# Kernel optimization log

Measured on AMD Instinct MI355X. Metric: run time of the kernel, lower is better.

## Reference

```python
import jax, jax.numpy as jnp
import numpy as np

EPS = 1e-5


def setup_inputs() -> dict:
    key = jax.random.key(0)
    ks = jax.random.split(key, 5)
    b, c, L = 2, 512, 1024
    x = jax.random.normal(ks[0], (b, c, L), dtype=jnp.float32)
    gamma = jnp.ones((c,), dtype=jnp.float32)
    beta = jnp.zeros((c,), dtype=jnp.float32)
    w_qkv = jax.random.normal(ks[1], (3 * c, c), dtype=jnp.float32) * (1.0 / np.sqrt(c))
    b_qkv = jax.random.normal(ks[2], (3 * c,), dtype=jnp.float32) * 0.02
    # NOTE: original zero-inits proj_out; we use random weights for a
    # non-degenerate correctness baseline (same math, different init values).
    w_proj = jax.random.normal(ks[3], (c, c), dtype=jnp.float32) * (1.0 / np.sqrt(c))
    b_proj = jnp.zeros((c,), dtype=jnp.float32)
    return {"x": x, "gamma": gamma, "beta": beta, "w_qkv": w_qkv,
            "b_qkv": b_qkv, "w_proj": w_proj, "b_proj": b_proj, "num_heads": 8}


def reference(x, gamma, beta, w_qkv, b_qkv, w_proj, b_proj, num_heads):
    b, c, L = x.shape
    nh = int(num_heads)
    hd = c // nh
    # BatchNorm1d, training mode: stats over (batch, length) per channel
    mean = jnp.mean(x, axis=(0, 2), keepdims=True)
    var = jnp.mean((x - mean) ** 2, axis=(0, 2), keepdims=True)  # biased var
    xn = (x - mean) * jax.lax.rsqrt(var + EPS)
    xn = xn * gamma[None, :, None] + beta[None, :, None]
    # 1x1 conv == matmul over channel axis: (b, 3c, L)
    qkv = jnp.einsum('oc,bcl->bol', w_qkv, xn) + b_qkv[None, :, None]
    # Faithful (quirky) layout: (b, 3*nh, hd, L) -> (b, hd, L, 3*nh)
    qkv = qkv.reshape(b, 3 * nh, hd, L).transpose(0, 2, 3, 1)
    q, k, v = jnp.split(qkv, 3, axis=-1)  # each (b, hd, L, nh)
    scale = (3 * nh) ** (-0.5)  # original scales by qkv's last dim before chunk
    # scores: (b, hd, T, T) -- 'heads' axis is hd due to the layout quirk
    w = jax.nn.softmax(jnp.einsum('bhtd,bhfd->bhtf', q * scale, k), axis=-1)
    a = jnp.einsum('bhtf,bhfd->bhtd', w, v)  # (b, hd, L, nh)
    h = a.transpose(0, 3, 1, 2).reshape(b, c, L)
    h = jnp.einsum('oc,bcl->bol', w_proj, h) + b_proj[None, :, None]
    return x + h
```

## Files before the change

kernel.cpp:

```cpp
#include <hip/hip_runtime.h>
#include <hip/hip_bf16.h>
#include <cstddef>
#include <cstdint>

#define B_ 2
#define C_ 512
#define L_ 1024
#define NH_ 8
#define HD_ 64
#define OC_ 1536

typedef short short8 __attribute__((ext_vector_type(8)));
typedef short short4v __attribute__((ext_vector_type(4)));
typedef float f32x4 __attribute__((ext_vector_type(4)));
typedef __fp16 f16x4 __attribute__((ext_vector_type(4)));
typedef __fp16 f16x2 __attribute__((ext_vector_type(2)));

#if defined(__has_builtin)
#if __has_builtin(__builtin_amdgcn_exp2f)
#define FEXP2(x) __builtin_amdgcn_exp2f(x)
#endif
#endif
#ifndef FEXP2
#define FEXP2(x) exp2f(x)
#endif

__device__ inline float bf_bits_to_f32(unsigned short u) {
  union { unsigned u32; float f; } c; c.u32 = ((unsigned)u) << 16; return c.f;
}
__device__ inline short f32_to_bf_bits(float f) {
  union { float f; unsigned u; } c; c.f = f;
  return (short)((c.u + 0x7FFFu + ((c.u >> 16) & 1u)) >> 16);
}

__global__ __launch_bounds__(256) void prep_kernel(
    const float* __restrict__ x, const float* __restrict__ gamma,
    const float* __restrict__ beta, const float* __restrict__ w_qkv,
    const float* __restrict__ w_proj,
    float* __restrict__ s_out, float* __restrict__ t_out,
    short* __restrict__ wq16, short* __restrict__ wpp16)
{
  const int bid = blockIdx.x;
  const int tid = threadIdx.x;
  if (bid < 512) {
    const int ch = bid;
    const float* p0 = x + (size_t)ch * L_;
    const float* p1 = x + (size_t)(C_ + ch) * L_;
    float s1 = 0.f, s2 = 0.f;
    for (int i = tid; i < L_; i += 256) {
      float v = p0[i]; s1 += v; s2 += v * v;
      v = p1[i];       s1 += v; s2 += v * v;
    }
    #pragma unroll
    for (int off = 32; off > 0; off >>= 1) {
      s1 += __shfl_down(s1, off);
      s2 += __shfl_down(s2, off);
    }
    __shared__ float r1[4], r2[4];
    const int wid = tid >> 6, lane = tid & 63;
    if (lane == 0) { r1[wid] = s1; r2[wid] = s2; }
    __syncthreads();
    if (tid == 0) {
      const float S1 = r1[0] + r1[1] + r1[2] + r1[3];
      const float S2 = r2[0] + r2[1] + r2[2] + r2[3];
      const float invN = 1.f / (float)(B_ * L_);
      const float mean = S1 * invN;
      const float var  = S2 * invN - mean * mean;
      const float rstd = rsqrtf(var + 1e-5f);
      const float sc = gamma[ch] * rstd;
      s_out[ch] = sc;
      t_out[ch] = beta[ch] - mean * sc;
    }
  } else if (bid < 704) {
    const int base = (bid - 512) * 4096 + tid * 16;
    #pragma unroll
    for (int it = 0; it < 2; ++it) {
      const float4 a0 = *(const float4*)(w_qkv + base + it * 8);
      const float4 a1 = *(const float4*)(w_qkv + base + it * 8 + 4);
      short8 v;
      v[0] = f32_to_bf_bits(a0.x); v[1] = f32_to_bf_bits(a0.y);
      v[2] = f32_to_bf_bits(a0.z); v[3] = f32_to_bf_bits(a0.w);
      v[4] = f32_to_bf_bits(a1.x); v[5] = f32_to_bf_bits(a1.y);
      v[6] = f32_to_bf_bits(a1.z); v[7] = f32_to_bf_bits(a1.w);
      *(short8*)(wq16 + base + it * 8) = v;
    }
  } else {
    #pragma unroll
    for (int grp = 0; grp < 4; ++grp) {
      const int idx = (bid - 704) * 4096 + tid * 16 + grp * 4;
      const int o = idx >> 9, cp = idx & 511;
      short4v v;
      #pragma unroll
      for (int j = 0; j < 4; ++j) {
        const int c = ((cp + j) & 7) * 64 + ((cp + j) >> 3);
        v[j] = f32_to_bf_bits(w_proj[(size_t)o * C_ + c]);
      }
      *(short4v*)(wpp16 + (size_t)o * C_ + cp) = v;
    }
  }
}

__global__ __launch_bounds__(256) void xt_kernel(
    const float* __restrict__ x, const float* __restrict__ s,
    const float* __restrict__ t, short* __restrict__ xT)
{
  __shared__ float T[64][65];
  const int t0 = blockIdx.x * 64, c0 = blockIdx.y * 64, b = blockIdx.z;
  const int tid = threadIdx.x;
  const float* xp = x + (size_t)b * C_ * L_;
  #pragma unroll
  for (int it = 0; it < 16; ++it) {
    const int idx = it * 256 + tid;
    const int rr = idx >> 6, cc = idx & 63;
    T[rr][cc] = fmaf(xp[(size_t)(c0 + rr) * L_ + t0 + cc], s[c0 + rr], t[c0 + rr]);
  }
  __syncthreads();
  #pragma unroll
  for (int it = 0; it < 16; ++it) {
    const int idx = it * 256 + tid;
    const int cc = idx >> 6, rr = idx & 63;
    xT[((size_t)b * L_ + t0 + cc) * C_ + c0 + rr] = f32_to_bf_bits(T[rr][cc]);
  }
}

template <int MR, int NR, bool OUT_BF16>
__global__ __launch_bounds__(256) void gemm_bt16_kernel(
    const short* __restrict__ A, const short* __restrict__ B,
    const float* __restrict__ bias, const float* __restrict__ res,
    void* __restrict__ Cv, int M, int N, int K,
    size_t sB, size_t sC, size_t sR)
{
  constexpr int BM = MR * 32, BN = NR * 32;
  __shared__ short As[BM * 64];
  __shared__ short Bs[BN * 64];
  const int tid = threadIdx.x;
  const int l = tid & 63, w = tid >> 6;
  const int wr = w >> 1, wc = w & 1;
  const int ll = l & 15;
  const int n0 = blockIdx.x * BN, m0 = blockIdx.y * BM, bz = blockIdx.z;
  const short* Bg = B + (size_t)bz * sB;
  f32x4 acc[MR][NR] = {};

  for (int k0 = 0; k0 < K; k0 += 64) {
    #pragma unroll
    for (int it = 0; it < BM / 32; ++it) {
      const int i = it * 256 + tid;
      const int row = i >> 3, s = i & 7;
      const short8 va = *(const short8*)(A + (size_t)(m0 + row) * K + k0 + s * 8);
      *(short8*)(As + row * 64 + (s ^ (row & 7)) * 8) = va;
    }
    #pragma unroll
    for (int it = 0; it < BN / 32; ++it) {
      const int i = it * 256 + tid;
      const int row = i >> 3, s = i & 7;
      const short8 vb = *(const short8*)(Bg + (size_t)(n0 + row) * K + k0 + s * 8);
      *(short8*)(Bs + row * 64 + (s ^ (row & 7)) * 8) = vb;
    }
    __syncthreads();
    #pragma unroll
    for (int kk = 0; kk < 2; ++kk) {
      short8 af[MR], bfg[NR];
      const int sd = kk * 4 + (l >> 4);
      #pragma unroll
      for (int m = 0; m < MR; ++m) {
        const int ra = wr * MR * 16 + m * 16 + ll;
        af[m] = *(const short8*)(As + ra * 64 + (sd ^ (ra & 7)) * 8);
      }
      #pragma unroll
      for (int n = 0; n < NR; ++n) {
        const int rb = wc * NR * 16 + n * 16 + ll;
        bfg[n] = *(const short8*)(Bs + rb * 64 + (sd ^ (rb & 7)) * 8);
      }
      #pragma unroll
      for (int m = 0; m < MR; ++m)
        #pragma unroll
        for (int n = 0; n < NR; ++n)
          acc[m][n] = __builtin_amdgcn_mfma_f32_16x16x32_bf16(
              af[m], bfg[n], acc[m][n], 0, 0, 0);
    }
    __syncthreads();
  }

  const int rg4 = (l >> 4) * 4;
  __hip_bfloat16* Cb = (__hip_bfloat16*)Cv + (size_t)bz * sC;
  float* Cf = (float*)Cv + (size_t)bz * sC;
  const float* Rp = res + (size_t)bz * sR;
  #pragma unroll
  for (int m = 0; m < MR; ++m) {
    #pragma unroll
    for (int reg = 0; reg < 4; ++reg) {
      const int gm = m0 + wr * MR * 16 + m * 16 + rg4 + reg;
      const float bv = bias[gm];
      #pragma unroll
      for (int n = 0; n < NR; ++n) {
        const int gn = n0 + wc * NR * 16 + n * 16 + ll;
        float v = acc[m][n][reg] + bv;
        if (OUT_BF16) {
          Cb[(size_t)gm * N + gn] = __hip_bfloat16_raw{(unsigned short)f32_to_bf_bits(v)};
        } else {
          v += Rp[(size_t)gm * N + gn];
          Cf[(size_t)gm * N + gn] = v;
        }
      }
    }
  }
}

__global__ __launch_bounds__(256, 4) void attn_kernel(
    const __hip_bfloat16* __restrict__ qkv, short* __restrict__ hT)
{
  __shared__ short Klds[1024 * 8];
  __shared__ __fp16 Vlds[8 * 1024];

  const int tq = blockIdx.x, d = blockIdx.y, b = blockIdx.z;
  const int tid = threadIdx.x;
  const int w = tid >> 6, l = tid & 63;
  const int lh = l >> 4, ll = l & 15;
  const int t0 = tq * 128 + w * 32;
  const short* base = (const short*)qkv + (size_t)b * OC_ * L_;
  short* VldsS = (short*)Vlds;

  #pragma unroll
  for (int it = 0; it < 4; ++it) {
    const int f = it * 256 + tid;
    short8 kv;
    #pragma unroll
    for (int g = 0; g < 8; ++g)
      kv[g] = base[(size_t)((8 + g) * HD_ + d) * L_ + f];
    *(short8*)(Klds + f * 8) = kv;
  }
  #pragma unroll
  for (int it = 0; it < 4; ++it) {
    const int i = it * 256 + tid;
    const int g = i >> 7, fs = i & 127;
    const short8 v = *(const short8*)(
        base + (size_t)((16 + g) * HD_ + d) * L_ + fs * 8);
    unsigned u[4];
    #pragma unroll
    for (int e = 0; e < 4; ++e) {
      const f16x2 p = __builtin_amdgcn_cvt_pkrtz(
          bf_bits_to_f32((unsigned short)v[2 * e]),
          bf_bits_to_f32((unsigned short)v[2 * e + 1]));
      u[e] = __builtin_bit_cast(unsigned, p);
    }
    uint4 uu; uu.x = u[0]; uu.y = u[1]; uu.z = u[2]; uu.w = u[3];
    *(uint4*)(VldsS + g * 1024 + ((fs & ~15) + ((fs & 15) ^ g)) * 8) = uu;
  }

  short8 bQ[2] = {};
  if (l < 16) {
    #pragma unroll
    for (int tt = 0; tt < 2; ++tt) {
      const int t = t0 + tt * 16 + ll;
      short8 qv;
      #pragma unroll
      for (int g = 0; g < 8; ++g) {
        const float v = bf_bits_to_f32(
            (unsigned short)base[(size_t)(g * HD_ + d) * L_ + t]);
        qv[g] = f32_to_bf_bits(v * 0.29448889f);
      }
      bQ[tt] = qv;
    }
  }

  __syncthreads();

  f16x4 vone, vzero;
  vone[0] = (__fp16)1.f; vone[1] = (__fp16)1.f;
  vone[2] = (__fp16)1.f; vone[3] = (__fp16)1.f;
  vzero[0] = (__fp16)0.f; vzero[1] = (__fp16)0.f;
  vzero[2] = (__fp16)0.f; vzero[3] = (__fp16)0.f;
  f32x4 accO[2] = {};

  for (int c = 0; c < 8; ++c) {
    short8 ak[8];
    #pragma unroll
    for (int ft = 0; ft < 8; ++ft)
      ak[ft] = *(const short8*)(Klds + (size_t)(c * 128 + ft * 16 + ll) * 8);
    f16x4 av[8];
    #pragma unroll
    for (int ft = 0; ft < 8; ++ft) {
      const int s16 = ft * 2 + (lh >> 1);
      const f16x4 raw = *(const f16x4*)(
          Vlds + (l & 7) * 1024 + c * 128 + ((s16 ^ (l & 7)) * 8) + (lh & 1) * 4);
      av[ft] = (ll < 8) ? raw : ((ll == 8) ? vone : vzero);
    }
    #pragma unroll
    for (int ft = 0; ft < 8; ++ft) {
      #pragma unroll
      for (int tt = 0; tt < 2; ++tt) {
        const f32x4 s = __builtin_amdgcn_mfma_f32_16x16x32_bf16(
            ak[ft], bQ[tt], (f32x4){0.f, 0.f, 0.f, 0.f}, 0, 0, 0);
        const f16x2 p0 = __builtin_amdgcn_cvt_pkrtz(FEXP2(s[0]), FEXP2(s[1]));
        const f16x2 p1 = __builtin_amdgcn_cvt_pkrtz(FEXP2(s[2]), FEXP2(s[3]));
        union { f16x4 v; uint2 u; } bp;
        bp.u.x = __builtin_bit_cast(unsigned, p0);
        bp.u.y = __builtin_bit_cast(unsigned, p1);
        accO[tt] = __builtin_amdgcn_mfma_f32_16x16x16f16(av[ft], bp.v, accO[tt], 0, 0, 0);
      }
    }
  }

  __syncthreads();
  short* Olds = Klds;
  #pragma unroll
  for (int nt = 0; nt < 2; ++nt) {
    const float sum = __shfl(accO[nt][0], 32 + ll);
    const float inv = 1.f / sum;
    if (lh < 2) {
      const int tl = w * 32 + nt * 16 + ll;
      #pragma unroll
      for (int reg = 0; reg < 4; ++reg)
        Olds[tl * 8 + lh * 4 + reg] = f32_to_bf_bits(accO[nt][reg] * inv);
    }
  }
  __syncthreads();
  if (tid < 128) {
    const short8 ov = *(const short8*)(Olds + tid * 8);
    *(short8*)(hT + ((size_t)b * L_ + tq * 128 + tid) * C_ + d * 8) = ov;
  }
}

extern "C" void kernel_launch(void* const* d_in, const int* in_sizes, int n_in,
                              void* d_out, int out_size, void* d_ws, size_t ws_size,
                              hipStream_t stream) {
  (void)in_sizes; (void)n_in; (void)out_size; (void)ws_size;
  const float* x      = (const float*)d_in[0];
  const float* gamma  = (const float*)d_in[1];
  const float* beta   = (const float*)d_in[2];
  const float* w_qkv  = (const float*)d_in[3];
  const float* b_qkv  = (const float*)d_in[4];
  const float* w_proj = (const float*)d_in[5];
  const float* b_proj = (const float*)d_in[6];
  float* out = (float*)d_out;
  char* wsb = (char*)d_ws;

  float* s_buf = (float*)(wsb + 0);
  float* t_buf = (float*)(wsb + 2048);
  short* wq16  = (short*)(wsb + 4096);
  short* wpp16 = (short*)(wsb + 4096 + 1572864);
  short* xT    = (short*)(wsb + 4096 + 2097152);
  short* qkv   = (short*)(wsb + 4096 + 4194304);
  short* hT    = (short*)(wsb + 4096 + 10485760);

  hipLaunchKernelGGL(prep_kernel, dim3(768), dim3(256), 0, stream,
                     x, gamma, beta, w_qkv, w_proj, s_buf, t_buf, wq16, wpp16);
  hipLaunchKernelGGL(xt_kernel, dim3(L_ / 64, C_ / 64, B_), dim3(256), 0, stream,
                     x, s_buf, t_buf, xT);
  hipLaunchKernelGGL((gemm_bt16_kernel<2, 2, true>),
                     dim3(L_ / 64, OC_ / 64, B_), dim3(256), 0, stream,
                     wq16, xT, b_qkv, (const float*)nullptr, (void*)qkv,
                     OC_, L_, C_, (size_t)L_ * C_, (size_t)OC_ * L_, (size_t)0);
  hipLaunchKernelGGL(attn_kernel, dim3(8, HD_, B_), dim3(256), 0, stream,
                     (const __hip_bfloat16*)qkv, hT);
  hipLaunchKernelGGL((gemm_bt16_kernel<2, 2, false>),
                     dim3(L_ / 64, C_ / 64, B_), dim3(256), 0, stream,
                     wpp16, hT, b_proj, x, (void*)out,
                     C_, L_, C_, (size_t)L_ * C_, (size_t)C_ * L_, (size_t)C_ * L_);
}
```

Before: 53.52 us.

## Vectorize prep loads, use direct global-to-LDS loads in GEMM, retile projection GEMM

The BatchNorm statistics pass and the normalize-and-transpose kernel now use float4 loads and 4-wide bf16 stores instead of scalar accesses. The GEMM tile loads use global_load_lds to copy 16 bytes per lane straight into swizzled shared memory, skipping the round trip through registers. The attention kernel keeps a row of fp16 ones in LDS so the V fragment is a plain load rather than a per-lane select. The output projection GEMM switches to a 32-row tile to launch more blocks. Lanes 9-15 now read the ones row instead of zeros, which only affects accumulator rows that appear unused, and the direct LDS loads depend on the compiler inserting correct waits.

Measured after the change: 49.18 us. 1.09x faster.

```diff
diff --git a/kernel.cpp b/kernel.cpp
--- a/kernel.cpp
+++ b/kernel.cpp
@@ -31,6 +31,12 @@
 __device__ inline short f32_to_bf_bits(float f) {
   union { float f; unsigned u; } c; c.f = f;
   return (short)((c.u + 0x7FFFu + ((c.u >> 16) & 1u)) >> 16);
+}
+
+__device__ __forceinline__ void gl2lds16(const short* g, short* l) {
+  __builtin_amdgcn_global_load_lds(
+      (const __attribute__((address_space(1))) unsigned*)(const void*)g,
+      (__attribute__((address_space(3))) unsigned*)(void*)l, 16, 0, 0);
 }
 
 __global__ __launch_bounds__(256) void prep_kernel(
@@ -44,13 +50,11 @@
   const int tid = threadIdx.x;
   if (bid < 512) {
     const int ch = bid;
-    const float* p0 = x + (size_t)ch * L_;
-    const float* p1 = x + (size_t)(C_ + ch) * L_;
-    float s1 = 0.f, s2 = 0.f;
-    for (int i = tid; i < L_; i += 256) {
-      float v = p0[i]; s1 += v; s2 += v * v;
-      v = p1[i];       s1 += v; s2 += v * v;
-    }
+    const float4 v0 = *(const float4*)(x + (size_t)ch * L_ + tid * 4);
+    const float4 v1 = *(const float4*)(x + (size_t)(C_ + ch) * L_ + tid * 4);
+    float s1 = v0.x + v0.y + v0.z + v0.w + v1.x + v1.y + v1.z + v1.w;
+    float s2 = v0.x*v0.x + v0.y*v0.y + v0.z*v0.z + v0.w*v0.w
+             + v1.x*v1.x + v1.y*v1.y + v1.z*v1.z + v1.w*v1.w;
     #pragma unroll
     for (int off = 32; off > 0; off >>= 1) {
       s1 += __shfl_down(s1, off);
@@ -109,17 +113,25 @@
   const int tid = threadIdx.x;
   const float* xp = x + (size_t)b * C_ * L_;
   #pragma unroll
-  for (int it = 0; it < 16; ++it) {
+  for (int it = 0; it < 4; ++it) {
     const int idx = it * 256 + tid;
-    const int rr = idx >> 6, cc = idx & 63;
-    T[rr][cc] = fmaf(xp[(size_t)(c0 + rr) * L_ + t0 + cc], s[c0 + rr], t[c0 + rr]);
+    const int rr = idx >> 4, c4 = (idx & 15) * 4;
+    const float4 v = *(const float4*)(xp + (size_t)(c0 + rr) * L_ + t0 + c4);
+    const float sc = s[c0 + rr], tc = t[c0 + rr];
+    T[rr][c4 + 0] = fmaf(v.x, sc, tc);
+    T[rr][c4 + 1] = fmaf(v.y, sc, tc);
+    T[rr][c4 + 2] = fmaf(v.z, sc, tc);
+    T[rr][c4 + 3] = fmaf(v.w, sc, tc);
   }
   __syncthreads();
   #pragma unroll
-  for (int it = 0; it < 16; ++it) {
+  for (int it = 0; it < 4; ++it) {
     const int idx = it * 256 + tid;
-    const int cc = idx >> 6, rr = idx & 63;
-    xT[((size_t)b * L_ + t0 + cc) * C_ + c0 + rr] = f32_to_bf_bits(T[rr][cc]);
+    const int tt_ = idx >> 4, cc4 = (idx & 15) * 4;
+    short4v o;
+    #pragma unroll
+    for (int j = 0; j < 4; ++j) o[j] = f32_to_bf_bits(T[cc4 + j][tt_]);
+    *(short4v*)(xT + ((size_t)b * L_ + t0 + tt_) * C_ + c0 + cc4) = o;
   }
 }
 
@@ -144,17 +156,17 @@
   for (int k0 = 0; k0 < K; k0 += 64) {
     #pragma unroll
     for (int it = 0; it < BM / 32; ++it) {
-      const int i = it * 256 + tid;
-      const int row = i >> 3, s = i & 7;
-      const short8 va = *(const short8*)(A + (size_t)(m0 + row) * K + k0 + s * 8);
-      *(short8*)(As + row * 64 + (s ^ (row & 7)) * 8) = va;
+      const int row0 = w * (BM / 4) + it * 8;
+      const int row = row0 + (l >> 3), sl = l & 7;
+      gl2lds16(A + (size_t)(m0 + row) * K + k0 + ((sl ^ (row & 7)) * 8),
+               As + row0 * 64);
     }
     #pragma unroll
     for (int it = 0; it < BN / 32; ++it) {
-      const int i = it * 256 + tid;
-      const int row = i >> 3, s = i & 7;
-      const short8 vb = *(const short8*)(Bg + (size_t)(n0 + row) * K + k0 + s * 8);
-      *(short8*)(Bs + row * 64 + (s ^ (row & 7)) * 8) = vb;
+      const int row0 = w * (BN / 4) + it * 8;
+      const int row = row0 + (l >> 3), sl = l & 7;
+      gl2lds16(Bg + (size_t)(n0 + row) * K + k0 + ((sl ^ (row & 7)) * 8),
+               Bs + row0 * 64);
     }
     __syncthreads();
     #pragma unroll
@@ -210,7 +222,7 @@
     const __hip_bfloat16* __restrict__ qkv, short* __restrict__ hT)
 {
   __shared__ short Klds[1024 * 8];
-  __shared__ __fp16 Vlds[8 * 1024];
+  __shared__ __fp16 Vlds[9 * 1024];
 
   const int tq = blockIdx.x, d = blockIdx.y, b = blockIdx.z;
   const int tid = threadIdx.x;
@@ -246,6 +258,10 @@
     uint4 uu; uu.x = u[0]; uu.y = u[1]; uu.z = u[2]; uu.w = u[3];
     *(uint4*)(VldsS + g * 1024 + ((fs & ~15) + ((fs & 15) ^ g)) * 8) = uu;
   }
+  {
+    uint2 ones; ones.x = 0x3C003C00u; ones.y = 0x3C003C00u;
+    *(uint2*)(VldsS + 8 * 1024 + tid * 4) = ones;
+  }
 
   short8 bQ[2] = {};
   if (l < 16) {
@@ -265,11 +281,7 @@
 
   __syncthreads();
 
-  f16x4 vone, vzero;
-  vone[0] = (__fp16)1.f; vone[1] = (__fp16)1.f;
-  vone[2] = (__fp16)1.f; vone[3] = (__fp16)1.f;
-  vzero[0] = (__fp16)0.f; vzero[1] = (__fp16)0.f;
-  vzero[2] = (__fp16)0.f; vzero[3] = (__fp16)0.f;
+  const int vrow = (ll < 9) ? ll : 8;
   f32x4 accO[2] = {};
 
   for (int c = 0; c < 8; ++c) {
@@ -281,9 +293,8 @@
     #pragma unroll
     for (int ft = 0; ft < 8; ++ft) {
       const int s16 = ft * 2 + (lh >> 1);
-      const f16x4 raw = *(const f16x4*)(
-          Vlds + (l & 7) * 1024 + c * 128 + ((s16 ^ (l & 7)) * 8) + (lh & 1) * 4);
-      av[ft] = (ll < 8) ? raw : ((ll == 8) ? vone : vzero);
+      av[ft] = *(const f16x4*)(
+          Vlds + vrow * 1024 + c * 128 + ((s16 ^ (vrow & 7)) * 8) + (lh & 1) * 4);
     }
     #pragma unroll
     for (int ft = 0; ft < 8; ++ft) {
@@ -353,8 +364,8 @@
                      OC_, L_, C_, (size_t)L_ * C_, (size_t)OC_ * L_, (size_t)0);
   hipLaunchKernelGGL(attn_kernel, dim3(8, HD_, B_), dim3(256), 0, stream,
                      (const __hip_bfloat16*)qkv, hT);
-  hipLaunchKernelGGL((gemm_bt16_kernel<2, 2, false>),
-                     dim3(L_ / 64, C_ / 64, B_), dim3(256), 0, stream,
+  hipLaunchKernelGGL((gemm_bt16_kernel<1, 2, false>),
+                     dim3(L_ / 64, C_ / 32, B_), dim3(256), 0, stream,
                      wpp16, hT, b_proj, x, (void*)out,
                      C_, L_, C_, (size_t)L_ * C_, (size_t)C_ * L_, (size_t)C_ * L_);
 }
```
